# Kernel optimization log

Measured on AMD Instinct MI355X. Metric: run time of the kernel, lower is better.

## Reference

```python
import jax, jax.numpy as jnp
import numpy as np

B, T, C = 2, 2048, 1024
H, D = 16, 64


def setup_inputs() -> dict:
    key = jax.random.key(0)
    k1, k2, k3 = jax.random.split(key, 3)
    x = jax.random.normal(k1, (B, T, C), dtype=jnp.float32)
    w_qkv = jax.random.normal(k2, (C, 3 * H * D), dtype=jnp.float32) * (C ** -0.5)
    w_proj = jax.random.normal(k3, (H * D, C), dtype=jnp.float32) * ((H * D) ** -0.5)
    sink_logit = jnp.zeros((H,), dtype=jnp.float32)
    return {"x": x, "w_qkv": w_qkv, "w_proj": w_proj, "sink_logit": sink_logit}


def reference(x, w_qkv, w_proj, sink_logit):
    b, t, c = x.shape
    qkv = x @ w_qkv                                  # [B,T,3HD]
    q, k, v = jnp.split(qkv, 3, axis=-1)
    # [B,H,T,D]
    q = q.reshape(b, t, H, D).transpose(0, 2, 1, 3)
    k = k.reshape(b, t, H, D).transpose(0, 2, 1, 3)
    v = v.reshape(b, t, H, D).transpose(0, 2, 1, 3)

    scale = 1.0 / jnp.sqrt(jnp.asarray(D, dtype=x.dtype))
    scores = jnp.einsum('bhqd,bhkd->bhqk', q, k) * scale   # [B,H,T,T]
    neg_inf = jnp.finfo(x.dtype).min
    causal = jnp.tril(jnp.ones((t, t), dtype=bool))
    scores = jnp.where(causal[None, None], scores, neg_inf)

    # sink column: per-head learnable logit b (added post-scale, V is zero)
    sink = jnp.broadcast_to(sink_logit.reshape(1, H, 1, 1), (b, H, t, 1)).astype(x.dtype)
    aug = jnp.concatenate([sink, scores], axis=-1)          # [B,H,T,T+1]
    attn = jax.nn.softmax(aug, axis=-1)
    # sink V is zero, so drop the sink column for the value contraction
    y = jnp.einsum('bhqk,bhkd->bhqd', attn[..., 1:], v)     # [B,H,T,D]
    y = y.transpose(0, 2, 1, 3).reshape(b, t, H * D)
    return y @ w_proj
```

## Files before the change

kernel.cpp:

```cpp
#include <hip/hip_runtime.h>
#include <hip/hip_bf16.h>
#include <stdint.h>

#define B_ 2
#define T_ 2048
#define C_ 1024
#define H_ 16
#define D_ 64

typedef __attribute__((ext_vector_type(8))) short short8;
typedef __attribute__((ext_vector_type(4))) float floatx4;

__device__ __forceinline__ float bf2f(uint16_t b) {
    return __uint_as_float(((uint32_t)b) << 16);
}
__device__ __forceinline__ uint16_t f2b(float f) {
    __hip_bfloat16 h = __float2bfloat16(f);
    return *(uint16_t*)&h;
}
__device__ __forceinline__ float exp2v(float x) {
    float r;
    asm("v_exp_f32 %0, %1" : "=v"(r) : "v"(x));
    return r;
}
__device__ __forceinline__ uint32_t cvtpk(float lo, float hi) {
    uint32_t r;
    asm("v_cvt_pk_bf16_f32 %0, %1, %2" : "=v"(r) : "v"(lo), "v"(hi));
    return r;
}
__device__ __forceinline__ void glds16(const uint16_t* g, uint16_t* l) {
    __builtin_amdgcn_global_load_lds(
        (const __attribute__((address_space(1))) uint32_t*)g,
        (__attribute__((address_space(3))) uint32_t*)l, 16, 0, 0);
}

__global__ void prep(const float* __restrict__ x, uint16_t* __restrict__ x_c,
                     const float* __restrict__ w_qkv, uint16_t* __restrict__ wt_qkv,
                     const float* __restrict__ w_proj, uint16_t* __restrict__ wt_proj) {
    __shared__ uint16_t tile[64][65];
    int id = blockIdx.x;
    int tid = threadIdx.x;
    if (id < 4096) {
        int i = (id * 256 + tid) * 4;
        float4 v = *(const float4*)(x + i);
        x_c[i + 0] = f2b(v.x);
        x_c[i + 1] = f2b(v.y);
        x_c[i + 2] = f2b(v.z);
        x_c[i + 3] = f2b(v.w);
        return;
    }
    const float* in;
    uint16_t* out;
    int R, W, bx, by;
    if (id < 4864) {
        int tb = id - 4096;
        in = w_qkv; out = wt_qkv; R = 1024; W = 3072;
        bx = tb % 48; by = tb / 48;
    } else {
        int tb = id - 4864;
        in = w_proj; out = wt_proj; R = 1024; W = 1024;
        bx = tb & 15; by = tb >> 4;
    }
    int tx = tid & 63, ty = tid >> 6;
    int c0 = bx * 64, r0 = by * 64;
    #pragma unroll
    for (int i = 0; i < 64; i += 4)
        tile[ty + i][tx] = f2b(in[(size_t)(r0 + ty + i) * W + (c0 + tx)]);
    __syncthreads();
    #pragma unroll
    for (int i = 0; i < 64; i += 4)
        out[(size_t)(c0 + ty + i) * R + (r0 + tx)] = tile[tx][ty + i];
}

template <bool OUT_F32, int BN>
__global__ __launch_bounds__(256, 3)
void gemm_bt(const uint16_t* __restrict__ A, const uint16_t* __restrict__ Bt,
             void* __restrict__ Cv, int M, int N, int K) {
    constexpr int NJ = BN / 32;
    constexpr int BUFB = BN * 32;
    __shared__ uint16_t As[3][128][32];
    __shared__ uint16_t Bs[3][BN][32];
    int tid = threadIdx.x;
    int w = tid >> 6, lane = tid & 63;
    int quad = lane >> 4, l16 = lane & 15;
    int wr = (w >> 1) * 64, wc = (w & 1) * (BN / 2);

    int nwg = gridDim.x;
    int wg = (blockIdx.x & 7) * (nwg >> 3) + (blockIdx.x >> 3);
    int nby = N / BN;
    int row0 = (wg / nby) * 128;
    int col0 = (wg % nby) * BN;

    int sr = w * 32 + (lane >> 2);
    int gscA = ((lane & 3) ^ ((lane >> 2) & 3)) * 8;
    uint16_t* lA0 = &As[0][sr][(lane & 3) * 8];
    const uint16_t* gA = A + (size_t)(row0 + sr) * K + gscA;
    int srB = (BN == 128) ? sr : (tid >> 2);
    int gscB = ((lane & 3) ^ (srB & 3)) * 8;
    uint16_t* lB0 = &Bs[0][srB][(lane & 3) * 8];
    const uint16_t* gB = Bt + (size_t)(col0 + srB) * K + gscB;

    floatx4 acc[4][NJ];
    #pragma unroll
    for (int i = 0; i < 4; i++)
        #pragma unroll
        for (int j = 0; j < NJ; j++)
            acc[i][j] = (floatx4){0.f, 0.f, 0.f, 0.f};

#define STAGE3_(bs_, t_)                                                    \
    {                                                                       \
        const uint16_t* ga_ = gA + (size_t)(t_) * 32;                       \
        const uint16_t* gb_ = gB + (size_t)(t_) * 32;                       \
        uint16_t* la_ = lA0 + (bs_) * 4096;                                 \
        uint16_t* lb_ = lB0 + (bs_) * BUFB;                                 \
        glds16(ga_, la_);                                                   \
        glds16(ga_ + 16 * K, la_ + 512);                                    \
        glds16(gb_, lb_);                                                   \
        if constexpr (BN == 128) glds16(gb_ + 16 * K, lb_ + 512);           \
    }

    int NT = K >> 5;
    STAGE3_(0, 0);
    STAGE3_(1, 1);
    if constexpr (BN == 128)
        asm volatile("s_waitcnt vmcnt(4)" ::: "memory");
    else
        asm volatile("s_waitcnt vmcnt(3)" ::: "memory");
    __builtin_amdgcn_s_barrier();

    const uint16_t* Ab = &As[0][0][0];
    const uint16_t* Bb = &Bs[0][0][0];
    int s = (quad ^ (l16 & 3)) * 8;
    int bc = 0, bs = 2;
    for (int t = 0; t < NT; ++t) {
        if (t + 2 < NT) STAGE3_(bs, t + 2);
        const uint16_t* Ac = Ab + bc * 4096;
        const uint16_t* Bc = Bb + bc * BUFB;
        short8 af[4], bfr[NJ];
        #pragma unroll
        for (int i = 0; i < 4; i++)
            af[i] = *(const short8*)&Ac[(wr + i * 16 + l16) * 32 + s];
        #pragma unroll
        for (int j = 0; j < NJ; j++)
            bfr[j] = *(const short8*)&Bc[(wc + j * 16 + l16) * 32 + s];
        #pragma unroll
        for (int i = 0; i < 4; i++)
            #pragma unroll
            for (int j = 0; j < NJ; j++)
                acc[i][j] = __builtin_amdgcn_mfma_f32_16x16x32_bf16(
                    af[i], bfr[j], acc[i][j], 0, 0, 0);
        if (t + 2 < NT) {
            if constexpr (BN == 128)
                asm volatile("s_waitcnt vmcnt(4)" ::: "memory");
            else
                asm volatile("s_waitcnt vmcnt(3)" ::: "memory");
        } else {
            asm volatile("s_waitcnt vmcnt(0)" ::: "memory");
        }
        __builtin_amdgcn_s_barrier();
        bc = (bc == 2) ? 0 : bc + 1;
        bs = (bs == 2) ? 0 : bs + 1;
    }
#undef STAGE3_

    #pragma unroll
    for (int i = 0; i < 4; i++) {
        #pragma unroll
        for (int j = 0; j < NJ; j++) {
            int rbase = row0 + wr + i * 16 + quad * 4;
            int cg = col0 + wc + j * 16 + l16;
            #pragma unroll
            for (int r = 0; r < 4; r++) {
                if (OUT_F32)
                    ((float*)Cv)[(size_t)(rbase + r) * N + cg] = acc[i][j][r];
                else
                    ((uint16_t*)Cv)[(size_t)(rbase + r) * N + cg] = f2b(acc[i][j][r]);
            }
        }
    }
}

__global__ __launch_bounds__(256, 3)
void attn_mfma(const uint16_t* __restrict__ qkv,
               const float* __restrict__ sink,
               uint16_t* __restrict__ y) {
    __shared__ uint16_t Ks[2][64][72];
    __shared__ uint16_t Vt[2][64][72];
    __shared__ uint16_t Pl[4][16][72];

    int tid = threadIdx.x;
    int w = tid >> 6, lane = tid & 63;
    int quad = lane >> 4, l16 = lane & 15;

    int id = blockIdx.x;
    int strip = 31 - (id >> 5);
    int bh = id & 31;
    int b = bh >> 4, h = bh & 15;
    int q0 = strip * 64 + w * 16;
    int ktiles = strip + 1;

    const uint16_t* qkv_b = qkv + (size_t)b * T_ * 3072;

    const float QSC = 0.125f * 1.44269504f;
    short8 qf[2];
    {
        int qrow = q0 + l16;
        #pragma unroll
        for (int kd = 0; kd < 2; kd++) {
            uint4 raw = *(const uint4*)(qkv_b + (size_t)qrow * 3072 + h * 64 +
                                        kd * 32 + quad * 8);
            const uint16_t* rp = (const uint16_t*)&raw;
            short8 f;
            #pragma unroll
            for (int j = 0; j < 8; j++)
                f[j] = (short)f2b(bf2f(rp[j]) * QSC);
            qf[kd] = f;
        }
    }

    float m_s = sink[h] * 1.44269504f;
    float l_s = 1.0f;
    floatx4 acc_o[4];
    #pragma unroll
    for (int dt = 0; dt < 4; dt++)
        acc_o[dt] = (floatx4){0.f, 0.f, 0.f, 0.f};

    int t2 = tid >> 3;
    int dg = tid & 7;
    const uint16_t* kgp = qkv_b + 1024 + h * 64 + (size_t)(2 * t2) * 3072 + dg * 8;
    const uint16_t* vgp = kgp + 1024;
    int vcw = 2 * (t2 ^ (4 * dg));

    uint4 kr0 = *(const uint4*)(kgp);
    uint4 kr1 = *(const uint4*)(kgp + 3072);
    uint4 vr0 = *(const uint4*)(vgp);
    uint4 vr1 = *(const uint4*)(vgp + 3072);
    {
        *(uint4*)&Ks[0][2 * t2][dg * 8] = kr0;
        *(uint4*)&Ks[0][2 * t2 + 1][dg * 8] = kr1;
        const uint16_t* a0 = (const uint16_t*)&vr0;
        const uint16_t* a1 = (const uint16_t*)&vr1;
        #pragma unroll
        for (int j = 0; j < 8; j++)
            *(uint32_t*)&Vt[0][dg * 8 + j][vcw] =
                (uint32_t)a0[j] | ((uint32_t)a1[j] << 16);
    }
    if (ktiles > 1) {
        kr0 = *(const uint4*)(kgp + 64 * 3072);
        kr1 = *(const uint4*)(kgp + 64 * 3072 + 3072);
        vr0 = *(const uint4*)(vgp + 64 * 3072);
        vr1 = *(const uint4*)(vgp + 64 * 3072 + 3072);
    }
    __syncthreads();

    for (int kt = 0; kt < ktiles; kt++) {
        int cur = kt & 1;
        if (kt + 1 < ktiles) {
            *(uint4*)&Ks[cur ^ 1][2 * t2][dg * 8] = kr0;
            *(uint4*)&Ks[cur ^ 1][2 * t2 + 1][dg * 8] = kr1;
            const uint16_t* a0 = (const uint16_t*)&vr0;
            const uint16_t* a1 = (const uint16_t*)&vr1;
            #pragma unroll
            for (int j = 0; j < 8; j++)
                *(uint32_t*)&Vt[cur ^ 1][dg * 8 + j][vcw] =
                    (uint32_t)a0[j] | ((uint32_t)a1[j] << 16);
        }
        if (kt + 2 < ktiles) {
            size_t off = (size_t)(kt + 2) * 64 * 3072;
            kr0 = *(const uint4*)(kgp + off);
            kr1 = *(const uint4*)(kgp + off + 3072);
            vr0 = *(const uint4*)(vgp + off);
            vr1 = *(const uint4*)(vgp + off + 3072);
        }
        short8 kf[4][2];
        #pragma unroll
        for (int rt = 0; rt < 4; rt++) {
            kf[rt][0] = *(const short8*)&Ks[cur][rt * 16 + l16][quad * 8];
            kf[rt][1] = *(const short8*)&Ks[cur][rt * 16 + l16][32 + quad * 8];
        }
        short8 vf[2][4];
        #pragma unroll
        for (int kb = 0; kb < 2; kb++)
            #pragma unroll
            for (int dt = 0; dt < 4; dt++) {
                int d = dt * 16 + l16;
                int col = 2 * (((kb * 16) + quad * 4) ^ (4 * (d >> 3)));
                vf[kb][dt] = *(const short8*)&Vt[cur][d][col];
            }
        floatx4 acc_s[4];
        #pragma unroll
        for (int rt = 0; rt < 4; rt++)
            acc_s[rt] = (floatx4){0.f, 0.f, 0.f, 0.f};
        #pragma unroll
        for (int rt = 0; rt < 4; rt++) {
            acc_s[rt] = __builtin_amdgcn_mfma_f32_16x16x32_bf16(
                kf[rt][0], qf[0], acc_s[rt], 0, 0, 0);
            acc_s[rt] = __builtin_amdgcn_mfma_f32_16x16x32_bf16(
                kf[rt][1], qf[1], acc_s[rt], 0, 0, 0);
        }
        if (kt == strip) {
            int qg = q0 + l16;
            #pragma unroll
            for (int rt = 0; rt < 4; rt++) {
                int kg = kt * 64 + rt * 16 + quad * 4;
                #pragma unroll
                for (int r = 0; r < 4; r++)
                    if (kg + r > qg) acc_s[rt][r] = -1e30f;
            }
        }
        float mx = -1e30f;
        #pragma unroll
        for (int rt = 0; rt < 4; rt++)
            #pragma unroll
            for (int r = 0; r < 4; r++) mx = fmaxf(mx, acc_s[rt][r]);
        mx = fmaxf(mx, __shfl_xor(mx, 16));
        mx = fmaxf(mx, __shfl_xor(mx, 32));
        float mold = m_s;
        if (!__all(mx <= mold + 8.0f)) {
            float mnew = fmaxf(mold, mx);
            float alpha = exp2v(mold - mnew);
            m_s = mnew;
            l_s *= alpha;
            #pragma unroll
            for (int r = 0; r < 4; r++) {
                float ar = __shfl(alpha, (lane & 48) | (quad * 4 + r));
                #pragma unroll
                for (int dt = 0; dt < 4; dt++) acc_o[dt][r] *= ar;
            }
        }
        float mcur = m_s;
        float psum = 0.f;
        #pragma unroll
        for (int rt = 0; rt < 4; rt++) {
            float p0 = exp2v(acc_s[rt][0] - mcur);
            float p1 = exp2v(acc_s[rt][1] - mcur);
            float p2 = exp2v(acc_s[rt][2] - mcur);
            float p3 = exp2v(acc_s[rt][3] - mcur);
            psum += (p0 + p1) + (p2 + p3);
            uint2 pk;
            pk.x = cvtpk(p0, p1);
            pk.y = cvtpk(p2, p3);
            *(uint2*)&Pl[w][l16][rt * 16 + quad * 4] = pk;
        }
        psum += __shfl_xor(psum, 16);
        psum += __shfl_xor(psum, 32);
        l_s += psum;
        #pragma unroll
        for (int kb = 0; kb < 2; kb++) {
            short8 pf = *(const short8*)&Pl[w][l16][kb * 32 + quad * 8];
            #pragma unroll
            for (int dt = 0; dt < 4; dt++)
                acc_o[dt] = __builtin_amdgcn_mfma_f32_16x16x32_bf16(
                    pf, vf[kb][dt], acc_o[dt], 0, 0, 0);
        }
        __syncthreads();
    }

    #pragma unroll
    for (int r = 0; r < 4; r++) {
        float lr = __shfl(l_s, (lane & 48) | (quad * 4 + r));
        float inv = 1.0f / lr;
        int qg = q0 + quad * 4 + r;
        uint16_t* yp = y + (size_t)(b * T_ + qg) * 1024 + h * 64;
        #pragma unroll
        for (int dt = 0; dt < 4; dt++)
            yp[dt * 16 + l16] = f2b(acc_o[dt][r] * inv);
    }
}

extern "C" void kernel_launch(void* const* d_in, const int* in_sizes, int n_in,
                              void* d_out, int out_size, void* d_ws, size_t ws_size,
                              hipStream_t stream) {
    const float* x      = (const float*)d_in[0];
    const float* w_qkv  = (const float*)d_in[1];
    const float* w_proj = (const float*)d_in[2];
    const float* sink   = (const float*)d_in[3];
    float* out          = (float*)d_out;

    char* ws = (char*)d_ws;
    uint16_t* wt_qkv  = (uint16_t*)ws;
    uint16_t* wt_proj = (uint16_t*)(ws + 6291456);
    uint16_t* x_c     = (uint16_t*)(ws + 8388608);
    uint16_t* qkv     = (uint16_t*)(ws + 16777216);
    uint16_t* yb      = (uint16_t*)(ws + 41943040);

    prep<<<dim3(5120), 256, 0, stream>>>(x, x_c, w_qkv, wt_qkv, w_proj, wt_proj);

    gemm_bt<false, 128><<<dim3(768), 256, 0, stream>>>(
        x_c, wt_qkv, qkv, 4096, 3072, 1024);

    attn_mfma<<<dim3(32 * 32), 256, 0, stream>>>(qkv, sink, yb);

    gemm_bt<true, 64><<<dim3(512), 256, 0, stream>>>(
        yb, wt_proj, out, 4096, 1024, 1024);
}
```

Measured before the change: 177.7 us.

## Fuse prep, QKV GEMM, attention and projection into one persistent kernel

```diff
diff --git a/kernel.cpp b/kernel.cpp
--- a/kernel.cpp
+++ b/kernel.cpp
@@ -7,6 +7,7 @@
 #define C_ 1024
 #define H_ 16
 #define D_ 64
+#define NBLK 768
 
 typedef __attribute__((ext_vector_type(8))) short short8;
 typedef __attribute__((ext_vector_type(4))) float floatx4;
@@ -34,59 +35,34 @@
         (__attribute__((address_space(3))) uint32_t*)l, 16, 0, 0);
 }
 
-__global__ void prep(const float* __restrict__ x, uint16_t* __restrict__ x_c,
-                     const float* __restrict__ w_qkv, uint16_t* __restrict__ wt_qkv,
-                     const float* __restrict__ w_proj, uint16_t* __restrict__ wt_proj) {
-    __shared__ uint16_t tile[64][65];
-    int id = blockIdx.x;
-    int tid = threadIdx.x;
-    if (id < 4096) {
-        int i = (id * 256 + tid) * 4;
-        float4 v = *(const float4*)(x + i);
-        x_c[i + 0] = f2b(v.x);
-        x_c[i + 1] = f2b(v.y);
-        x_c[i + 2] = f2b(v.z);
-        x_c[i + 3] = f2b(v.w);
-        return;
-    }
-    const float* in;
-    uint16_t* out;
-    int R, W, bx, by;
-    if (id < 4864) {
-        int tb = id - 4096;
-        in = w_qkv; out = wt_qkv; R = 1024; W = 3072;
-        bx = tb % 48; by = tb / 48;
-    } else {
-        int tb = id - 4864;
-        in = w_proj; out = wt_proj; R = 1024; W = 1024;
-        bx = tb & 15; by = tb >> 4;
-    }
-    int tx = tid & 63, ty = tid >> 6;
-    int c0 = bx * 64, r0 = by * 64;
-    #pragma unroll
-    for (int i = 0; i < 64; i += 4)
-        tile[ty + i][tx] = f2b(in[(size_t)(r0 + ty + i) * W + (c0 + tx)]);
+__device__ __forceinline__ void gbar(uint32_t* c) {
     __syncthreads();
-    #pragma unroll
-    for (int i = 0; i < 64; i += 4)
-        out[(size_t)(c0 + ty + i) * R + (r0 + tx)] = tile[tx][ty + i];
+    if (threadIdx.x == 0) {
+        __threadfence();
+        __hip_atomic_fetch_add(c, 1u, __ATOMIC_ACQ_REL, __HIP_MEMORY_SCOPE_AGENT);
+        while (__hip_atomic_load(c, __ATOMIC_ACQUIRE, __HIP_MEMORY_SCOPE_AGENT) <
+               (uint32_t)NBLK)
+            __builtin_amdgcn_s_sleep(2);
+        __threadfence();
+    }
+    __syncthreads();
 }
 
 template <bool OUT_F32, int BN>
-__global__ __launch_bounds__(256, 3)
-void gemm_bt(const uint16_t* __restrict__ A, const uint16_t* __restrict__ Bt,
-             void* __restrict__ Cv, int M, int N, int K) {
+__device__ void gemm_phase(const uint16_t* __restrict__ A,
+                           const uint16_t* __restrict__ Bt,
+                           void* __restrict__ Cv, int N, int K,
+                           int wgid, int nwg, char* smem) {
     constexpr int NJ = BN / 32;
     constexpr int BUFB = BN * 32;
-    __shared__ uint16_t As[3][128][32];
-    __shared__ uint16_t Bs[3][BN][32];
+    uint16_t (*As)[128][32] = (uint16_t(*)[128][32])smem;
+    uint16_t (*Bs)[BN][32]  = (uint16_t(*)[BN][32])(smem + 24576);
     int tid = threadIdx.x;
     int w = tid >> 6, lane = tid & 63;
     int quad = lane >> 4, l16 = lane & 15;
     int wr = (w >> 1) * 64, wc = (w & 1) * (BN / 2);
 
-    int nwg = gridDim.x;
-    int wg = (blockIdx.x & 7) * (nwg >> 3) + (blockIdx.x >> 3);
+    int wg = (wgid & 7) * (nwg >> 3) + (wgid >> 3);
     int nby = N / BN;
     int row0 = (wg / nby) * 128;
     int col0 = (wg % nby) * BN;
@@ -180,19 +156,17 @@
     }
 }
 
-__global__ __launch_bounds__(256, 3)
-void attn_mfma(const uint16_t* __restrict__ qkv,
-               const float* __restrict__ sink,
-               uint16_t* __restrict__ y) {
-    __shared__ uint16_t Ks[2][64][72];
-    __shared__ uint16_t Vt[2][64][72];
-    __shared__ uint16_t Pl[4][16][72];
+__device__ void attn_phase(const uint16_t* __restrict__ qkv,
+                           const float* __restrict__ sink,
+                           uint16_t* __restrict__ y, int id, char* smem) {
+    uint16_t (*Ks)[64][72] = (uint16_t(*)[64][72])smem;
+    uint16_t (*Vt)[64][72] = (uint16_t(*)[64][72])(smem + 18432);
+    uint16_t (*Pl)[16][72] = (uint16_t(*)[16][72])(smem + 36864);
 
     int tid = threadIdx.x;
     int w = tid >> 6, lane = tid & 63;
     int quad = lane >> 4, l16 = lane & 15;
 
-    int id = blockIdx.x;
     int strip = 31 - (id >> 5);
     int bh = id & 31;
     int b = bh >> 4, h = bh & 15;
@@ -368,6 +342,68 @@
     }
 }
 
+__global__ __launch_bounds__(256, 3)
+void fused(const float* __restrict__ x, const float* __restrict__ w_qkv,
+           const float* __restrict__ w_proj, const float* __restrict__ sink,
+           float* __restrict__ out, uint16_t* __restrict__ wt_qkv,
+           uint16_t* __restrict__ wt_proj, uint16_t* __restrict__ xc_yb,
+           uint16_t* __restrict__ qkv, uint32_t* __restrict__ bar) {
+    __shared__ __align__(16) char smem[49152];
+    int tid = threadIdx.x;
+    int bid = blockIdx.x;
+
+    for (int id = bid; id < 5120; id += NBLK) {
+        if (id < 4096) {
+            int i = (id * 256 + tid) * 4;
+            float4 v = *(const float4*)(x + i);
+            xc_yb[i + 0] = f2b(v.x);
+            xc_yb[i + 1] = f2b(v.y);
+            xc_yb[i + 2] = f2b(v.z);
+            xc_yb[i + 3] = f2b(v.w);
+        } else {
+            uint16_t (*tile)[65] = (uint16_t(*)[65])smem;
+            const float* in;
+            uint16_t* op;
+            int R, W, bx, by;
+            if (id < 4864) {
+                int tb = id - 4096;
+                in = w_qkv; op = wt_qkv; R = 1024; W = 3072;
+                bx = tb % 48; by = tb / 48;
+            } else {
+                int tb = id - 4864;
+                in = w_proj; op = wt_proj; R = 1024; W = 1024;
+                bx = tb & 15; by = tb >> 4;
+            }
+            int tx = tid & 63, ty = tid >> 6;
+            int c0 = bx * 64, r0 = by * 64;
+            __syncthreads();
+            #pragma unroll
+            for (int i = 0; i < 64; i += 4)
+                tile[ty + i][tx] = f2b(in[(size_t)(r0 + ty + i) * W + (c0 + tx)]);
+            __syncthreads();
+            #pragma unroll
+            for (int i = 0; i < 64; i += 4)
+                op[(size_t)(c0 + ty + i) * R + (r0 + tx)] = tile[tx][ty + i];
+        }
+    }
+    gbar(bar + 0);
+
+    gemm_phase<false, 128>(xc_yb, wt_qkv, qkv, 3072, 1024, bid, 768, smem);
+    gbar(bar + 1);
+
+    if (bid < 256) {
+        attn_phase(qkv, sink, xc_yb, bid, smem);
+        __syncthreads();
+        attn_phase(qkv, sink, xc_yb, 1023 - bid, smem);
+    } else {
+        attn_phase(qkv, sink, xc_yb, bid, smem);
+    }
+    gbar(bar + 2);
+
+    if (bid < 512)
+        gemm_phase<true, 64>(xc_yb, wt_proj, out, 1024, 1024, bid, 512, smem);
+}
+
 extern "C" void kernel_launch(void* const* d_in, const int* in_sizes, int n_in,
                               void* d_out, int out_size, void* d_ws, size_t ws_size,
                               hipStream_t stream) {
@@ -380,17 +416,11 @@
     char* ws = (char*)d_ws;
     uint16_t* wt_qkv  = (uint16_t*)ws;
     uint16_t* wt_proj = (uint16_t*)(ws + 6291456);
-    uint16_t* x_c     = (uint16_t*)(ws + 8388608);
-    uint16_t* qkv     = (uint16_t*)(ws + 16777216);
-    uint16_t* yb      = (uint16_t*)(ws + 41943040);
-
-    prep<<<dim3(5120), 256, 0, stream>>>(x, x_c, w_qkv, wt_qkv, w_proj, wt_proj);
-
-    gemm_bt<false, 128><<<dim3(768), 256, 0, stream>>>(
-        x_c, wt_qkv, qkv, 4096, 3072, 1024);
-
-    attn_mfma<<<dim3(32 * 32), 256, 0, stream>>>(qkv, sink, yb);
-
-    gemm_bt<true, 64><<<dim3(512), 256, 0, stream>>>(
-        yb, wt_proj, out, 4096, 1024, 1024);
-}
+    uint16_t* xc_yb   = (uint16_t*)(ws + 8388608);
+    uint16_t* qkvb    = (uint16_t*)(ws + 16777216);
+    uint32_t* bar     = (uint32_t*)(ws + 41943040);
+
+    hipMemsetAsync(bar, 0, 64, stream);
+    fused<<<dim3(NBLK), 256, 0, stream>>>(x, w_qkv, w_proj, sink, out,
+                                          wt_qkv, wt_proj, xc_yb, qkvb, bar);
+}
```

Result: slower. 667.5 us (+275.6%).

## Add large-tile 256x192 QKV GEMM kernel with 512 threads and asymmetric buffering

Applied to the files above, without the earlier changes.

```diff
diff --git a/kernel.cpp b/kernel.cpp
--- a/kernel.cpp
+++ b/kernel.cpp
@@ -72,6 +72,108 @@
         out[(size_t)(c0 + ty + i) * R + (r0 + tx)] = tile[tx][ty + i];
 }
 
+__global__ __launch_bounds__(512, 1)
+void gemm_qkv(const uint16_t* __restrict__ A, const uint16_t* __restrict__ Bt,
+              uint16_t* __restrict__ C, int M, int N, int K) {
+    __shared__ uint16_t As[3][256][64];
+    __shared__ uint16_t Bs[2][192][64];
+    int tid = threadIdx.x;
+    int w = tid >> 6, lane = tid & 63;
+    int quad = lane >> 4, l16 = lane & 15;
+    int wm = w >> 2, wn = w & 3;
+
+    int wg = (blockIdx.x & 7) * 32 + (blockIdx.x >> 3);
+    int row0 = (wg >> 4) * 256;
+    int col0 = (wg & 15) * 192;
+
+    int srA = w * 32 + (lane >> 3);
+    int srB = w * 24 + (lane >> 3);
+    int gsc = ((lane & 7) ^ ((lane >> 3) & 7)) * 8;
+    uint16_t* lA0 = &As[0][srA][(lane & 7) * 8];
+    uint16_t* lB0 = &Bs[0][srB][(lane & 7) * 8];
+    const uint16_t* gA = A + (size_t)(row0 + srA) * K + gsc;
+    const uint16_t* gB = Bt + (size_t)(col0 + srB) * K + gsc;
+
+    floatx4 acc[8][3];
+    #pragma unroll
+    for (int i = 0; i < 8; i++)
+        #pragma unroll
+        for (int j = 0; j < 3; j++)
+            acc[i][j] = (floatx4){0.f, 0.f, 0.f, 0.f};
+
+#define STAGEA_(b_, t_)                                                     \
+    {                                                                       \
+        const uint16_t* g_ = gA + (size_t)(t_) * 64;                        \
+        uint16_t* l_ = lA0 + (b_) * (256 * 64);                             \
+        _Pragma("unroll") for (int g = 0; g < 4; g++)                       \
+            glds16(g_ + (size_t)g * 8 * K, l_ + g * 8 * 64);                \
+    }
+#define STAGEB_(b_, t_)                                                     \
+    {                                                                       \
+        const uint16_t* g_ = gB + (size_t)(t_) * 64;                        \
+        uint16_t* l_ = lB0 + (b_) * (192 * 64);                             \
+        _Pragma("unroll") for (int g = 0; g < 3; g++)                       \
+            glds16(g_ + (size_t)g * 8 * K, l_ + g * 8 * 64);                \
+    }
+
+    int NT = K >> 6;
+    STAGEA_(0, 0);
+    STAGEB_(0, 0);
+    STAGEA_(1, 1);
+    asm volatile("s_waitcnt vmcnt(4)" ::: "memory");
+    __builtin_amdgcn_s_barrier();
+
+    int sA = (l16 & 7);
+    for (int t = 0; t < NT; ++t) {
+        int bufA = t % 3, bufB = t & 1;
+        if (t + 1 < NT) STAGEB_(bufB ^ 1, t + 1);
+        if (t + 2 < NT) STAGEA_((t + 2) % 3, t + 2);
+        short8 bfr[3][2];
+        #pragma unroll
+        for (int j = 0; j < 3; j++)
+            #pragma unroll
+            for (int kk = 0; kk < 2; kk++)
+                bfr[j][kk] = *(const short8*)&Bs[bufB][wn * 48 + j * 16 + l16]
+                                               [((kk * 4 + quad) ^ sA) * 8];
+        __builtin_amdgcn_s_setprio(1);
+        #pragma unroll
+        for (int i = 0; i < 8; i++) {
+            short8 af0 = *(const short8*)&As[bufA][wm * 128 + i * 16 + l16]
+                                            [((0 + quad) ^ sA) * 8];
+            short8 af1 = *(const short8*)&As[bufA][wm * 128 + i * 16 + l16]
+                                            [((4 + quad) ^ sA) * 8];
+            #pragma unroll
+            for (int j = 0; j < 3; j++) {
+                acc[i][j] = __builtin_amdgcn_mfma_f32_16x16x32_bf16(
+                    af0, bfr[j][0], acc[i][j], 0, 0, 0);
+                acc[i][j] = __builtin_amdgcn_mfma_f32_16x16x32_bf16(
+                    af1, bfr[j][1], acc[i][j], 0, 0, 0);
+            }
+        }
+        __builtin_amdgcn_s_setprio(0);
+        if (t + 2 < NT) {
+            asm volatile("s_waitcnt vmcnt(4)" ::: "memory");
+        } else if (t + 1 < NT) {
+            asm volatile("s_waitcnt vmcnt(0)" ::: "memory");
+        }
+        __builtin_amdgcn_s_barrier();
+    }
+#undef STAGEA_
+#undef STAGEB_
+
+    #pragma unroll
+    for (int i = 0; i < 8; i++) {
+        #pragma unroll
+        for (int j = 0; j < 3; j++) {
+            int rbase = row0 + wm * 128 + i * 16 + quad * 4;
+            int cg = col0 + wn * 48 + j * 16 + l16;
+            #pragma unroll
+            for (int r = 0; r < 4; r++)
+                C[(size_t)(rbase + r) * N + cg] = f2b(acc[i][j][r]);
+        }
+    }
+}
+
 template <bool OUT_F32, int BN>
 __global__ __launch_bounds__(256, 3)
 void gemm_bt(const uint16_t* __restrict__ A, const uint16_t* __restrict__ Bt,
@@ -386,8 +488,7 @@
 
     prep<<<dim3(5120), 256, 0, stream>>>(x, x_c, w_qkv, wt_qkv, w_proj, wt_proj);
 
-    gemm_bt<false, 128><<<dim3(768), 256, 0, stream>>>(
-        x_c, wt_qkv, qkv, 4096, 3072, 1024);
+    gemm_qkv<<<dim3(256), 512, 0, stream>>>(x_c, wt_qkv, qkv, 4096, 3072, 1024);
 
     attn_mfma<<<dim3(32 * 32), 256, 0, stream>>>(qkv, sink, yb);
 
```

Result: no change. 177.4 us (-0.2%).
